# Optimization experiments

Hardware: AMD Instinct MI355X
Metric: run time of the kernel (lower is better)

The kernel has to match this reference:

```python
import jax, jax.numpy as jnp
import numpy as np

N0, N1, N2 = 100000, 50000, 20000
D = 128
E0, E1 = 600000, 300000


def _sage_rel(x_src, x_dst, src, dst, Ws, Wn, b, n_dst):
    """DGL SAGEConv(mean): fc_self(x_dst) + fc_neigh(mean of in-neighbors) + b."""
    msg = x_src[src]                                              # [E, D] gather
    ssum = jax.ops.segment_sum(msg, dst, num_segments=n_dst)      # [n_dst, D]
    deg = jax.ops.segment_sum(jnp.ones(dst.shape, x_src.dtype), dst, num_segments=n_dst)
    h_neigh = ssum / jnp.maximum(deg, 1.0)[:, None]               # zero-degree -> 0
    return x_dst @ Ws + h_neigh @ Wn + b


def setup_inputs() -> dict:
    key = jax.random.key(0)
    ks = jax.random.split(key, 24)
    p = 0.05
    inp = {
        "x": jax.random.normal(ks[0], (N0, D), jnp.float32),
        "e0_src_r0": jax.random.randint(ks[1], (E0,), 0, N0),
        "e0_dst_r0": jax.random.randint(ks[2], (E0,), 0, N1),
        "e0_src_r1": jax.random.randint(ks[3], (E0,), 0, N0),
        "e0_dst_r1": jax.random.randint(ks[4], (E0,), 0, N1),
        "e1_src_r0": jax.random.randint(ks[5], (E1,), 0, N1),
        "e1_dst_r0": jax.random.randint(ks[6], (E1,), 0, N2),
        "e1_src_r1": jax.random.randint(ks[7], (E1,), 0, N1),
        "e1_dst_r1": jax.random.randint(ks[8], (E1,), 0, N2),
    }
    names = ["Ws1_r0", "Wn1_r0", "Ws1_r1", "Wn1_r1", "Ws2_r0", "Wn2_r0", "Ws2_r1", "Wn2_r1"]
    for i, n in enumerate(names):
        inp[n] = jax.random.normal(ks[9 + i], (D, D), jnp.float32) * p
    for i, n in enumerate(["b1_r0", "b1_r1", "b2_r0", "b2_r1"]):
        inp[n] = jax.random.normal(ks[17 + i], (D,), jnp.float32) * p
    return inp


def reference(x, e0_src_r0, e0_dst_r0, e0_src_r1, e0_dst_r1,
              e1_src_r0, e1_dst_r0, e1_src_r1, e1_dst_r1,
              Ws1_r0, Wn1_r0, b1_r0, Ws1_r1, Wn1_r1, b1_r1,
              Ws2_r0, Wn2_r0, b2_r0, Ws2_r1, Wn2_r1, b2_r1):
    # Layer 1: HeteroGraphConv sum over relations, then ReLU
    x_dst1 = x[:N1]
    h1 = (_sage_rel(x, x_dst1, e0_src_r0, e0_dst_r0, Ws1_r0, Wn1_r0, b1_r0, N1)
          + _sage_rel(x, x_dst1, e0_src_r1, e0_dst_r1, Ws1_r1, Wn1_r1, b1_r1, N1))
    h1 = jax.nn.relu(h1)
    # Layer 2
    h1_dst = h1[:N2]
    h2 = (_sage_rel(h1, h1_dst, e1_src_r0, e1_dst_r0, Ws2_r0, Wn2_r0, b2_r0, N2)
          + _sage_rel(h1, h1_dst, e1_src_r1, e1_dst_r1, Ws2_r1, Wn2_r1, b2_r1, N2))
    return h2
```

## Files before the change

kernel.cpp:

```cpp
#include <hip/hip_runtime.h>
#include <hip/hip_bf16.h>

#define N0 100000
#define N1 50000
#define N2 20000
#define DD 128
#define E0 600000
#define E1 300000

#define NSEG_TOT (2 * N1 + 2 * N2)
#define ETOT     (2 * E0 + 2 * E1)

#define SEG_SHIFT 9
#define NBK  ((NSEG_TOT + 511) / 512)
#define NBK_PAD 288
#define CH   2048
#define NCH  ((ETOT + CH - 1) / CH)
#define CAP  13568

#define CAST_BLOCKS 12500
#define PREP_BLOCKS 48
#define CNT_BLOCKS  NCH
#define PROLOGUE_BLOCKS (CAST_BLOCKS + PREP_BLOCKS + CNT_BLOCKS)

typedef __attribute__((ext_vector_type(8))) short short8;
typedef __attribute__((ext_vector_type(4))) float floatx4;

__device__ __forceinline__ void st2bf(__hip_bfloat16* p, float a, float b) {
    __hip_bfloat162 v;
    v.x = __float2bfloat16(a);
    v.y = __float2bfloat16(b);
    *(__hip_bfloat162*)p = v;
}
__device__ __forceinline__ short bf16bits(float v) {
    __hip_bfloat16 b = __float2bfloat16(v);
    return *(short*)&b;
}
__device__ __forceinline__ float bf2f(unsigned short u) {
    return __uint_as_float(((unsigned int)u) << 16);
}
__device__ __forceinline__ float4 ld4bf(const __hip_bfloat16* p) {
    ushort4 u = *(const ushort4*)p;
    return make_float4(bf2f(u.x), bf2f(u.y), bf2f(u.z), bf2f(u.w));
}
__device__ __forceinline__ void st4bf(__hip_bfloat16* p, float4 v) {
    short vs[4];
    vs[0] = bf16bits(v.x); vs[1] = bf16bits(v.y);
    vs[2] = bf16bits(v.z); vs[3] = bf16bits(v.w);
    *(int2*)p = *(int2*)vs;
}

__device__ __forceinline__ int scan256(int s, int* sh, int t) {
    sh[t] = s;
    __syncthreads();
    for (int off = 1; off < 256; off <<= 1) {
        int tmp = (t >= off) ? sh[t - off] : 0;
        __syncthreads();
        sh[t] += tmp;
        __syncthreads();
    }
    return sh[t];
}

__device__ __forceinline__ int edge_seg(int e,
    const int* d0, const int* d1, const int* d2, const int* d3)
{
    if (e < E0)               return d0[e];
    if (e < 2 * E0)           return N1 + d1[e - E0];
    if (e < 2 * E0 + E1)      return 2 * N1 + d2[e - 2 * E0];
    return 2 * N1 + N2 + d3[e - 2 * E0 - E1];
}
__device__ __forceinline__ int2 edge_seg_src(int e,
    const int* s0, const int* d0, const int* s1, const int* d1,
    const int* s2, const int* d2, const int* s3, const int* d3)
{
    if (e < E0)               return make_int2(s0[e],            d0[e]);
    if (e < 2 * E0)           return make_int2(s1[e - E0],       N1 + d1[e - E0]);
    if (e < 2 * E0 + E1)      return make_int2(s2[e - 2 * E0],   2 * N1 + d2[e - 2 * E0]);
    int ee = e - 2 * E0 - E1;
    return make_int2(s3[ee], 2 * N1 + N2 + d3[ee]);
}

__global__ __launch_bounds__(256) void prologue_kernel(
    const float* __restrict__ x, __hip_bfloat16* __restrict__ xb,
    const int* __restrict__ d0a, const int* __restrict__ d0b,
    const int* __restrict__ d1a, const int* __restrict__ d1b,
    int* __restrict__ cntmat,
    const float* __restrict__ Ws1a, const float* __restrict__ Ws1b,
    const float* __restrict__ Wn1a, const float* __restrict__ Wn1b,
    const float* __restrict__ Ws2a, const float* __restrict__ Ws2b,
    const float* __restrict__ Wn2a, const float* __restrict__ Wn2b,
    short* __restrict__ wfrag1, short* __restrict__ wfrag2)
{
    __shared__ int hist[NBK_PAD];
    const int bid = blockIdx.x;
    const int t = threadIdx.x;
    if (bid < CAST_BLOCKS) {
        int i = bid * 256 + t;
        float4 v = ((const float4*)x)[i];
        st2bf(xb + (size_t)i * 4, v.x, v.y);
        st2bf(xb + (size_t)i * 4 + 2, v.z, v.w);
    } else if (bid < CAST_BLOCKS + PREP_BLOCKS) {
        int p = (bid - CAST_BLOCKS) * 256 + t;
        int layer = p >= 6144;
        int q = p - layer * 6144;
        int lane = q & 63;
        int mt = (q >> 6) & 7;
        int kc = q >> 9;
        int n = mt * 16 + (lane & 15);
        int k0 = kc * 32 + ((lane >> 4) << 3);
        const float* Wsa = layer ? Ws2a : Ws1a;
        const float* Wsb = layer ? Ws2b : Ws1b;
        const float* Wna = layer ? Wn2a : Wn1a;
        const float* Wnb = layer ? Wn2b : Wn1b;
        short* wf = layer ? wfrag2 : wfrag1;
        short vals[8];
#pragma unroll
        for (int j = 0; j < 8; j++) {
            int k = k0 + j;
            float w;
            if (k < 128)      w = Wsa[k * DD + n] + Wsb[k * DD + n];
            else if (k < 256) w = Wna[(k - 128) * DD + n];
            else              w = Wnb[(k - 256) * DD + n];
            vals[j] = bf16bits(w);
        }
        *(short8*)(wf + (size_t)q * 8) = *(short8*)vals;
    } else {
        const int chunk = bid - CAST_BLOCKS - PREP_BLOCKS;
        for (int l = t; l < NBK_PAD; l += 256) hist[l] = 0;
        __syncthreads();
#pragma unroll
        for (int it = 0; it < CH / 256; it++) {
            int e = chunk * CH + it * 256 + t;
            if (e < ETOT) {
                int seg = edge_seg(e, d0a, d0b, d1a, d1b);
                atomicAdd(&hist[seg >> SEG_SHIFT], 1);
            }
        }
        __syncthreads();
        for (int g = t; g < NBK; g += 256)
            cntmat[(size_t)g * NCH + chunk] = hist[g];
    }
}

__global__ __launch_bounds__(256) void scan_chunks_kernel(
    const int* __restrict__ cntmat, int* __restrict__ pre, int* __restrict__ tot)
{
    __shared__ int sh[256];
    const int t = threadIdx.x;
    const int g = blockIdx.x;
    const size_t roff = (size_t)g * NCH;
    int v[4]; int s = 0;
#pragma unroll
    for (int i = 0; i < 4; i++) {
        int idx = t * 4 + i;
        v[i] = (idx < NCH) ? cntmat[roff + idx] : 0;
        s += v[i];
    }
    int incl = scan256(s, sh, t);
    int ex = incl - s;
#pragma unroll
    for (int i = 0; i < 4; i++) {
        int idx = t * 4 + i;
        if (idx < NCH) pre[roff + idx] = ex;
        ex += v[i];
    }
    if (t == 255) tot[g] = incl;
}

__device__ __forceinline__ void build_base(const int* tot, int* basel, int* sh, int t)
{
    int l0 = 2 * t, l1 = 2 * t + 1;
    int v0 = (l0 < NBK) ? tot[l0] : 0;
    int v1 = (l1 < NBK) ? tot[l1] : 0;
    int s = v0 + v1;
    int incl = scan256(s, sh, t);
    int ex = incl - s;
    basel[l0] = ex;
    basel[l1] = ex + v0;
}

__global__ __launch_bounds__(256) void bucket_scatter_kernel(
    const int* __restrict__ s0a, const int* __restrict__ d0a,
    const int* __restrict__ s0b, const int* __restrict__ d0b,
    const int* __restrict__ s1a, const int* __restrict__ d1a,
    const int* __restrict__ s1b, const int* __restrict__ d1b,
    const int* __restrict__ pre, const int* __restrict__ tot,
    int2* __restrict__ ebuf)
{
    __shared__ int sh[256];
    __shared__ int basel[512];
    __shared__ int cur[NBK_PAD];
    const int t = threadIdx.x;
    const int chunk = blockIdx.x;

    build_base(tot, basel, sh, t);
    for (int l = t; l < NBK_PAD; l += 256) cur[l] = 0;
    __syncthreads();

#pragma unroll
    for (int it = 0; it < CH / 256; it++) {
        int e = chunk * CH + it * 256 + t;
        if (e < ETOT) {
            int2 r = edge_seg_src(e, s0a, d0a, s0b, d0b, s1a, d1a, s1b, d1b);
            int g = r.y >> SEG_SHIFT;
            int rk = atomicAdd(&cur[g], 1);
            int pos = basel[g] + pre[(size_t)g * NCH + chunk] + rk;
            ebuf[pos] = r;
        }
    }
}

__global__ __launch_bounds__(256) void csr_finalize_kernel(
    const int2* __restrict__ ebuf, const int* __restrict__ tot,
    int* __restrict__ row_ptr, int* __restrict__ eidx)
{
    __shared__ int sh[256];
    __shared__ int basel[512];
    __shared__ int cnt[512];
    __shared__ int excl[512];
    __shared__ int leidx[CAP];
    const int t = threadIdx.x;
    const int g = blockIdx.x;
    const int l0 = 2 * t, l1 = 2 * t + 1;

    build_base(tot, basel, sh, t);
    cnt[l0] = 0; cnt[l1] = 0;
    __syncthreads();

    const int b0 = basel[g];
    const int b1 = (g + 1 < 512) ? basel[g + 1] : ETOT;
    const int Eloc = b1 - b0;
    const int segbase = g << SEG_SHIFT;

    for (int i = t; i < Eloc; i += 256) {
        int2 rec = ebuf[b0 + i];
        atomicAdd(&cnt[rec.y - segbase], 1);
    }
    __syncthreads();

    int c0 = cnt[l0], c1 = cnt[l1];
    int ss = c0 + c1;
    int inc2 = scan256(ss, sh, t);
    int ex2 = inc2 - ss;
    excl[l0] = ex2;
    excl[l1] = ex2 + c0;
    __syncthreads();

    int nloc = NSEG_TOT - segbase;
    if (nloc > 512) nloc = 512;
    for (int l = t; l < nloc; l += 256) row_ptr[segbase + l] = b0 + excl[l];
    if (g == 0 && t == 0) row_ptr[NSEG_TOT] = ETOT;

    cnt[l0] = 0; cnt[l1] = 0;
    __syncthreads();

    if (Eloc <= CAP) {
        for (int i = t; i < Eloc; i += 256) {
            int2 rec = ebuf[b0 + i];
            int l = rec.y - segbase;
            int r = atomicAdd(&cnt[l], 1);
            leidx[excl[l] + r] = rec.x;
        }
        __syncthreads();
        for (int i = t; i < Eloc; i += 256) eidx[b0 + i] = leidx[i];
    } else {
        for (int i = t; i < Eloc; i += 256) {
            int2 rec = ebuf[b0 + i];
            int l = rec.y - segbase;
            int r = atomicAdd(&cnt[l], 1);
            eidx[b0 + excl[l] + r] = rec.x;
        }
    }
}

__global__ __launch_bounds__(256) void aggregate_kernel(
    const __hip_bfloat16* __restrict__ xb,
    const int* __restrict__ row_ptr,
    const int* __restrict__ eidx,
    __hip_bfloat16* __restrict__ hn,
    int nseg)
{
    int wid = (blockIdx.x * 256 + threadIdx.x) >> 6;
    const int lane = threadIdx.x & 63;
    if (wid >= nseg) return;
    wid = __builtin_amdgcn_readfirstlane(wid);

    const int beg = row_ptr[wid];
    const int end = row_ptr[wid + 1];
    const int cnt = end - beg;
    const int half = lane >> 5;
    const int l32 = lane & 31;

    float4 s = make_float4(0.f, 0.f, 0.f, 0.f);
    int k = beg;
    for (; k + 4 <= end; k += 4) {
        int i0 = eidx[k + 0];
        int i1 = eidx[k + 1];
        int i2 = eidx[k + 2];
        int i3 = eidx[k + 3];
        int ra = half ? i1 : i0;
        int rb = half ? i3 : i2;
        float4 va = ld4bf(xb + (long)ra * DD + l32 * 4);
        float4 vb = ld4bf(xb + (long)rb * DD + l32 * 4);
        s.x += va.x + vb.x; s.y += va.y + vb.y;
        s.z += va.z + vb.z; s.w += va.w + vb.w;
    }
    if (k + 2 <= end) {
        int i0 = eidx[k];
        int i1 = eidx[k + 1];
        int r = half ? i1 : i0;
        float4 v = ld4bf(xb + (long)r * DD + l32 * 4);
        s.x += v.x; s.y += v.y; s.z += v.z; s.w += v.w;
        k += 2;
    }
    if (k < end && !half) {
        int i0 = eidx[k];
        float4 v = ld4bf(xb + (long)i0 * DD + l32 * 4);
        s.x += v.x; s.y += v.y; s.z += v.z; s.w += v.w;
    }

    s.x += __shfl_xor(s.x, 32);
    s.y += __shfl_xor(s.y, 32);
    s.z += __shfl_xor(s.z, 32);
    s.w += __shfl_xor(s.w, 32);

    if (!half) {
        const float inv = 1.f / (float)(cnt > 1 ? cnt : 1);
        float4 m = make_float4(s.x * inv, s.y * inv, s.z * inv, s.w * inv);
        st4bf(hn + (long)wid * DD + l32 * 4, m);
    }
}

template <bool RELU, typename TOUT>
__global__ __launch_bounds__(256) void mfma_combine_kernel(
    const __hip_bfloat16* __restrict__ xself,
    const __hip_bfloat16* __restrict__ hn,
    const short* __restrict__ wfrag,
    const float* __restrict__ b0, const float* __restrict__ b1,
    TOUT* __restrict__ out, int M)
{
    const int t = threadIdx.x;
    const int wave = t >> 6;
    const int lane = t & 63;
    const int nsub = lane & 15;
    const int quad = lane >> 4;
    const int base = blockIdx.x * 128 + wave * 32;

    const int node0 = base + nsub;
    const int node1 = base + 16 + nsub;
    const long n0c = node0 < M ? node0 : M - 1;
    const long n1c = node1 < M ? node1 : M - 1;

    floatx4 acc[2][8];
#pragma unroll
    for (int nt = 0; nt < 2; nt++)
#pragma unroll
        for (int mt = 0; mt < 8; mt++) acc[nt][mt] = (floatx4){0.f, 0.f, 0.f, 0.f};

    for (int kc = 0; kc < 12; kc++) {
        const __hip_bfloat16* src;
        long r0, r1;
        int koff;
        if (kc < 4)      { src = xself; koff = kc * 32;       r0 = n0c;     r1 = n1c; }
        else if (kc < 8) { src = hn;    koff = (kc - 4) * 32; r0 = n0c;     r1 = n1c; }
        else             { src = hn;    koff = (kc - 8) * 32; r0 = M + n0c; r1 = M + n1c; }

        short8 bf0 = *(const short8*)(src + r0 * DD + koff + quad * 8);
        short8 bf1 = *(const short8*)(src + r1 * DD + koff + quad * 8);
        const short* wbase = wfrag + ((size_t)(kc * 8) * 64 + lane) * 8;
#pragma unroll
        for (int mt = 0; mt < 8; mt++) {
            short8 af = *(const short8*)(wbase + (size_t)mt * 64 * 8);
            acc[0][mt] = __builtin_amdgcn_mfma_f32_16x16x32_bf16(af, bf0, acc[0][mt], 0, 0, 0);
            acc[1][mt] = __builtin_amdgcn_mfma_f32_16x16x32_bf16(af, bf1, acc[1][mt], 0, 0, 0);
        }
    }

#pragma unroll
    for (int nt = 0; nt < 2; nt++) {
        int node = (nt == 0) ? node0 : node1;
        if (node >= M) continue;
#pragma unroll
        for (int mt = 0; mt < 8; mt++) {
            int c0 = mt * 16 + quad * 4;
            float4 bb0 = *(const float4*)(b0 + c0);
            float4 bb1 = *(const float4*)(b1 + c0);
            float v0 = acc[nt][mt][0] + bb0.x + bb1.x;
            float v1 = acc[nt][mt][1] + bb0.y + bb1.y;
            float v2 = acc[nt][mt][2] + bb0.z + bb1.z;
            float v3 = acc[nt][mt][3] + bb0.w + bb1.w;
            if (RELU) {
                v0 = v0 > 0.f ? v0 : 0.f;
                v1 = v1 > 0.f ? v1 : 0.f;
                v2 = v2 > 0.f ? v2 : 0.f;
                v3 = v3 > 0.f ? v3 : 0.f;
            }
            TOUT* p = out + (long)node * DD + c0;
            if constexpr (sizeof(TOUT) == 4) {
                *(float4*)p = make_float4(v0, v1, v2, v3);
            } else {
                short vs[4];
                vs[0] = bf16bits(v0); vs[1] = bf16bits(v1);
                vs[2] = bf16bits(v2); vs[3] = bf16bits(v3);
                *(int2*)p = *(int2*)vs;
            }
        }
    }
}


extern "C" void kernel_launch(void* const* d_in, const int* in_sizes, int n_in,
                              void* d_out, int out_size, void* d_ws, size_t ws_size,
                              hipStream_t stream)
{
    const float* x = (const float*)d_in[0];
    const int* e0_src_r0 = (const int*)d_in[1];
    const int* e0_dst_r0 = (const int*)d_in[2];
    const int* e0_src_r1 = (const int*)d_in[3];
    const int* e0_dst_r1 = (const int*)d_in[4];
    const int* e1_src_r0 = (const int*)d_in[5];
    const int* e1_dst_r0 = (const int*)d_in[6];
    const int* e1_src_r1 = (const int*)d_in[7];
    const int* e1_dst_r1 = (const int*)d_in[8];
    const float* Ws1_r0 = (const float*)d_in[9];
    const float* Wn1_r0 = (const float*)d_in[10];
    const float* Ws1_r1 = (const float*)d_in[11];
    const float* Wn1_r1 = (const float*)d_in[12];
    const float* Ws2_r0 = (const float*)d_in[13];
    const float* Wn2_r0 = (const float*)d_in[14];
    const float* Ws2_r1 = (const float*)d_in[15];
    const float* Wn2_r1 = (const float*)d_in[16];
    const float* b1_r0 = (const float*)d_in[17];
    const float* b1_r1 = (const float*)d_in[18];
    const float* b2_r0 = (const float*)d_in[19];
    const float* b2_r1 = (const float*)d_in[20];
    float* out = (float*)d_out;

    __hip_bfloat16* xb = (__hip_bfloat16*)d_ws;
    __hip_bfloat16* h1 = xb;
    __hip_bfloat16* hn = xb + (size_t)N0 * DD;
    int2* ebuf    = (int2*)hn;
    int* eidx     = (int*)(hn + (size_t)2 * N1 * DD);
    int* row_ptr  = eidx + ETOT;
    int* cntmat   = row_ptr + NSEG_TOT + 4;
    int* pre      = cntmat + NBK * NCH;
    int* tot      = pre + NBK * NCH;
    short* wfrag1 = (short*)(tot + NBK + 4);
    short* wfrag2 = wfrag1 + 12 * 8 * 64 * 8;

    prologue_kernel<<<PROLOGUE_BLOCKS, 256, 0, stream>>>(
        x, xb,
        e0_dst_r0, e0_dst_r1, e1_dst_r0, e1_dst_r1,
        cntmat,
        Ws1_r0, Ws1_r1, Wn1_r0, Wn1_r1,
        Ws2_r0, Ws2_r1, Wn2_r0, Wn2_r1,
        wfrag1, wfrag2);

    scan_chunks_kernel<<<NBK, 256, 0, stream>>>(cntmat, pre, tot);

    bucket_scatter_kernel<<<NCH, 256, 0, stream>>>(
        e0_src_r0, e0_dst_r0, e0_src_r1, e0_dst_r1,
        e1_src_r0, e1_dst_r0, e1_src_r1, e1_dst_r1,
        pre, tot, ebuf);

    csr_finalize_kernel<<<NBK, 256, 0, stream>>>(ebuf, tot, row_ptr, eidx);

    aggregate_kernel<<<(2 * N1 + 3) / 4, 256, 0, stream>>>(xb, row_ptr, eidx, hn, 2 * N1);
    mfma_combine_kernel<true, __hip_bfloat16>
        <<<(N1 + 127) / 128, 256, 0, stream>>>(xb, hn, wfrag1, b1_r0, b1_r1, h1, N1);

    aggregate_kernel<<<(2 * N2 + 3) / 4, 256, 0, stream>>>(h1, row_ptr + 2 * N1, eidx, hn, 2 * N2);
    mfma_combine_kernel<false, float>
        <<<(N2 + 127) / 128, 256, 0, stream>>>(h1, hn, wfrag2, b2_r0, b2_r1, out, N2);
}
```

Baseline: 297.1 us.

## Fuse CSR build into cooperative kernel and fuse aggregation with MFMA combine

Merges the prologue, chunk scan, bucket scatter and CSR finalize into one cooperative kernel with grid syncs, replacing four launches. It also fuses neighbor aggregation with the MFMA linear layer per layer, keeping mean features in LDS instead of writing and rereading them through global memory. The finalize step drops the LDS staging of eidx and writes scattered to global. The fused layer uses 64 nodes per block with one N-tile per wave, which halves weight reuse per fragment load, and grid syncs plus the fixed 1024-block grid may limit parallelism in the cast and scatter phases.

Result: slower. 828.1 us (+178.8%).

```diff
diff --git a/kernel.cpp b/kernel.cpp
--- a/kernel.cpp
+++ b/kernel.cpp
@@ -1,5 +1,8 @@
 #include <hip/hip_runtime.h>
+#include <hip/hip_cooperative_groups.h>
 #include <hip/hip_bf16.h>
+
+namespace cg = cooperative_groups;
 
 #define N0 100000
 #define N1 50000
@@ -16,12 +19,12 @@
 #define NBK_PAD 288
 #define CH   2048
 #define NCH  ((ETOT + CH - 1) / CH)
-#define CAP  13568
-
-#define CAST_BLOCKS 12500
-#define PREP_BLOCKS 48
-#define CNT_BLOCKS  NCH
-#define PROLOGUE_BLOCKS (CAST_BLOCKS + PREP_BLOCKS + CNT_BLOCKS)
+
+#define COOP_GRID 1024
+
+#define LNODES 64
+#define LROWS  (2 * LNODES)
+#define LSTRIDE 152
 
 typedef __attribute__((ext_vector_type(8))) short short8;
 typedef __attribute__((ext_vector_type(4))) float floatx4;
@@ -79,93 +82,6 @@
     if (e < 2 * E0 + E1)      return make_int2(s2[e - 2 * E0],   2 * N1 + d2[e - 2 * E0]);
     int ee = e - 2 * E0 - E1;
     return make_int2(s3[ee], 2 * N1 + N2 + d3[ee]);
-}
-
-__global__ __launch_bounds__(256) void prologue_kernel(
-    const float* __restrict__ x, __hip_bfloat16* __restrict__ xb,
-    const int* __restrict__ d0a, const int* __restrict__ d0b,
-    const int* __restrict__ d1a, const int* __restrict__ d1b,
-    int* __restrict__ cntmat,
-    const float* __restrict__ Ws1a, const float* __restrict__ Ws1b,
-    const float* __restrict__ Wn1a, const float* __restrict__ Wn1b,
-    const float* __restrict__ Ws2a, const float* __restrict__ Ws2b,
-    const float* __restrict__ Wn2a, const float* __restrict__ Wn2b,
-    short* __restrict__ wfrag1, short* __restrict__ wfrag2)
-{
-    __shared__ int hist[NBK_PAD];
-    const int bid = blockIdx.x;
-    const int t = threadIdx.x;
-    if (bid < CAST_BLOCKS) {
-        int i = bid * 256 + t;
-        float4 v = ((const float4*)x)[i];
-        st2bf(xb + (size_t)i * 4, v.x, v.y);
-        st2bf(xb + (size_t)i * 4 + 2, v.z, v.w);
-    } else if (bid < CAST_BLOCKS + PREP_BLOCKS) {
-        int p = (bid - CAST_BLOCKS) * 256 + t;
-        int layer = p >= 6144;
-        int q = p - layer * 6144;
-        int lane = q & 63;
-        int mt = (q >> 6) & 7;
-        int kc = q >> 9;
-        int n = mt * 16 + (lane & 15);
-        int k0 = kc * 32 + ((lane >> 4) << 3);
-        const float* Wsa = layer ? Ws2a : Ws1a;
-        const float* Wsb = layer ? Ws2b : Ws1b;
-        const float* Wna = layer ? Wn2a : Wn1a;
-        const float* Wnb = layer ? Wn2b : Wn1b;
-        short* wf = layer ? wfrag2 : wfrag1;
-        short vals[8];
-#pragma unroll
-        for (int j = 0; j < 8; j++) {
-            int k = k0 + j;
-            float w;
-            if (k < 128)      w = Wsa[k * DD + n] + Wsb[k * DD + n];
-            else if (k < 256) w = Wna[(k - 128) * DD + n];
-            else              w = Wnb[(k - 256) * DD + n];
-            vals[j] = bf16bits(w);
-        }
-        *(short8*)(wf + (size_t)q * 8) = *(short8*)vals;
-    } else {
-        const int chunk = bid - CAST_BLOCKS - PREP_BLOCKS;
-        for (int l = t; l < NBK_PAD; l += 256) hist[l] = 0;
-        __syncthreads();
-#pragma unroll
-        for (int it = 0; it < CH / 256; it++) {
-            int e = chunk * CH + it * 256 + t;
-            if (e < ETOT) {
-                int seg = edge_seg(e, d0a, d0b, d1a, d1b);
-                atomicAdd(&hist[seg >> SEG_SHIFT], 1);
-            }
-        }
-        __syncthreads();
-        for (int g = t; g < NBK; g += 256)
-            cntmat[(size_t)g * NCH + chunk] = hist[g];
-    }
-}
-
-__global__ __launch_bounds__(256) void scan_chunks_kernel(
-    const int* __restrict__ cntmat, int* __restrict__ pre, int* __restrict__ tot)
-{
-    __shared__ int sh[256];
-    const int t = threadIdx.x;
-    const int g = blockIdx.x;
-    const size_t roff = (size_t)g * NCH;
-    int v[4]; int s = 0;
-#pragma unroll
-    for (int i = 0; i < 4; i++) {
-        int idx = t * 4 + i;
-        v[i] = (idx < NCH) ? cntmat[roff + idx] : 0;
-        s += v[i];
-    }
-    int incl = scan256(s, sh, t);
-    int ex = incl - s;
-#pragma unroll
-    for (int i = 0; i < 4; i++) {
-        int idx = t * 4 + i;
-        if (idx < NCH) pre[roff + idx] = ex;
-        ex += v[i];
-    }
-    if (t == 255) tot[g] = incl;
 }
 
 __device__ __forceinline__ void build_base(const int* tot, int* basel, int* sh, int t)
@@ -180,216 +96,262 @@
     basel[l1] = ex + v0;
 }
 
-__global__ __launch_bounds__(256) void bucket_scatter_kernel(
-    const int* __restrict__ s0a, const int* __restrict__ d0a,
-    const int* __restrict__ s0b, const int* __restrict__ d0b,
-    const int* __restrict__ s1a, const int* __restrict__ d1a,
-    const int* __restrict__ s1b, const int* __restrict__ d1b,
-    const int* __restrict__ pre, const int* __restrict__ tot,
-    int2* __restrict__ ebuf)
-{
+struct CsrArgs {
+    const float* x; __hip_bfloat16* xb;
+    const int* s0a; const int* d0a; const int* s0b; const int* d0b;
+    const int* s1a; const int* d1a; const int* s1b; const int* d1b;
+    int* cntmat; int* pre; int* tot; int2* ebuf; int* row_ptr; int* eidx;
+    const float* Ws1a; const float* Ws1b; const float* Wn1a; const float* Wn1b;
+    const float* Ws2a; const float* Ws2b; const float* Wn2a; const float* Wn2b;
+    short* wfrag1; short* wfrag2;
+};
+
+__global__ __launch_bounds__(256, 4) void coop_csr_kernel(CsrArgs a)
+{
+    cg::grid_group grid = cg::this_grid();
     __shared__ int sh[256];
     __shared__ int basel[512];
-    __shared__ int cur[NBK_PAD];
+    __shared__ int hist[512];
+    __shared__ int excl[512];
     const int t = threadIdx.x;
-    const int chunk = blockIdx.x;
-
-    build_base(tot, basel, sh, t);
-    for (int l = t; l < NBK_PAD; l += 256) cur[l] = 0;
+    const int nthr = gridDim.x * 256;
+    const int gtid = blockIdx.x * 256 + t;
+
+    for (int i = gtid; i < N0 * DD / 4; i += nthr) {
+        float4 v = ((const float4*)a.x)[i];
+        st2bf(a.xb + (size_t)i * 4, v.x, v.y);
+        st2bf(a.xb + (size_t)i * 4 + 2, v.z, v.w);
+    }
+    for (int p = gtid; p < 2 * 6144; p += nthr) {
+        int layer = p >= 6144;
+        int q = p - layer * 6144;
+        int lane = q & 63;
+        int mt = (q >> 6) & 7;
+        int kc = q >> 9;
+        int n = mt * 16 + (lane & 15);
+        int k0 = kc * 32 + ((lane >> 4) << 3);
+        const float* Wsa = layer ? a.Ws2a : a.Ws1a;
+        const float* Wsb = layer ? a.Ws2b : a.Ws1b;
+        const float* Wna = layer ? a.Wn2a : a.Wn1a;
+        const float* Wnb = layer ? a.Wn2b : a.Wn1b;
+        short* wf = layer ? a.wfrag2 : a.wfrag1;
+        short vals[8];
+#pragma unroll
+        for (int j = 0; j < 8; j++) {
+            int k = k0 + j;
+            float w;
+            if (k < 128)      w = Wsa[k * DD + n] + Wsb[k * DD + n];
+            else if (k < 256) w = Wna[(k - 128) * DD + n];
+            else              w = Wnb[(k - 256) * DD + n];
+            vals[j] = bf16bits(w);
+        }
+        *(short8*)(wf + (size_t)q * 8) = *(short8*)vals;
+    }
+    for (int chunk = blockIdx.x; chunk < NCH; chunk += gridDim.x) {
+        for (int l = t; l < NBK_PAD; l += 256) hist[l] = 0;
+        __syncthreads();
+#pragma unroll
+        for (int it = 0; it < CH / 256; it++) {
+            int e = chunk * CH + it * 256 + t;
+            if (e < ETOT) {
+                int seg = edge_seg(e, a.d0a, a.d0b, a.d1a, a.d1b);
+                atomicAdd(&hist[seg >> SEG_SHIFT], 1);
+            }
+        }
+        __syncthreads();
+        for (int g = t; g < NBK; g += 256)
+            a.cntmat[(size_t)g * NCH + chunk] = hist[g];
+        __syncthreads();
+    }
+    grid.sync();
+
+    for (int g = blockIdx.x; g < NBK; g += gridDim.x) {
+        const size_t roff = (size_t)g * NCH;
+        int v[4]; int s = 0;
+#pragma unroll
+        for (int i = 0; i < 4; i++) {
+            int idx = t * 4 + i;
+            v[i] = (idx < NCH) ? a.cntmat[roff + idx] : 0;
+            s += v[i];
+        }
+        int incl = scan256(s, sh, t);
+        int ex = incl - s;
+#pragma unroll
+        for (int i = 0; i < 4; i++) {
+            int idx = t * 4 + i;
+            if (idx < NCH) a.pre[roff + idx] = ex;
+            ex += v[i];
+        }
+        if (t == 255) a.tot[g] = incl;
+        __syncthreads();
+    }
+    grid.sync();
+
+    build_base(a.tot, basel, sh, t);
     __syncthreads();
-
-#pragma unroll
-    for (int it = 0; it < CH / 256; it++) {
-        int e = chunk * CH + it * 256 + t;
-        if (e < ETOT) {
-            int2 r = edge_seg_src(e, s0a, d0a, s0b, d0b, s1a, d1a, s1b, d1b);
-            int g = r.y >> SEG_SHIFT;
-            int rk = atomicAdd(&cur[g], 1);
-            int pos = basel[g] + pre[(size_t)g * NCH + chunk] + rk;
-            ebuf[pos] = r;
-        }
-    }
-}
-
-__global__ __launch_bounds__(256) void csr_finalize_kernel(
-    const int2* __restrict__ ebuf, const int* __restrict__ tot,
-    int* __restrict__ row_ptr, int* __restrict__ eidx)
-{
-    __shared__ int sh[256];
-    __shared__ int basel[512];
-    __shared__ int cnt[512];
-    __shared__ int excl[512];
-    __shared__ int leidx[CAP];
-    const int t = threadIdx.x;
-    const int g = blockIdx.x;
+    for (int chunk = blockIdx.x; chunk < NCH; chunk += gridDim.x) {
+        for (int l = t; l < NBK_PAD; l += 256) hist[l] = 0;
+        __syncthreads();
+#pragma unroll
+        for (int it = 0; it < CH / 256; it++) {
+            int e = chunk * CH + it * 256 + t;
+            if (e < ETOT) {
+                int2 r = edge_seg_src(e, a.s0a, a.d0a, a.s0b, a.d0b,
+                                         a.s1a, a.d1a, a.s1b, a.d1b);
+                int g = r.y >> SEG_SHIFT;
+                int rk = atomicAdd(&hist[g], 1);
+                a.ebuf[basel[g] + a.pre[(size_t)g * NCH + chunk] + rk] = r;
+            }
+        }
+        __syncthreads();
+    }
+    grid.sync();
+
     const int l0 = 2 * t, l1 = 2 * t + 1;
-
-    build_base(tot, basel, sh, t);
-    cnt[l0] = 0; cnt[l1] = 0;
-    __syncthreads();
-
-    const int b0 = basel[g];
-    const int b1 = (g + 1 < 512) ? basel[g + 1] : ETOT;
-    const int Eloc = b1 - b0;
-    const int segbase = g << SEG_SHIFT;
-
-    for (int i = t; i < Eloc; i += 256) {
-        int2 rec = ebuf[b0 + i];
-        atomicAdd(&cnt[rec.y - segbase], 1);
-    }
-    __syncthreads();
-
-    int c0 = cnt[l0], c1 = cnt[l1];
-    int ss = c0 + c1;
-    int inc2 = scan256(ss, sh, t);
-    int ex2 = inc2 - ss;
-    excl[l0] = ex2;
-    excl[l1] = ex2 + c0;
-    __syncthreads();
-
-    int nloc = NSEG_TOT - segbase;
-    if (nloc > 512) nloc = 512;
-    for (int l = t; l < nloc; l += 256) row_ptr[segbase + l] = b0 + excl[l];
-    if (g == 0 && t == 0) row_ptr[NSEG_TOT] = ETOT;
-
-    cnt[l0] = 0; cnt[l1] = 0;
-    __syncthreads();
-
-    if (Eloc <= CAP) {
+    for (int g = blockIdx.x; g < NBK; g += gridDim.x) {
+        hist[l0] = 0; hist[l1] = 0;
+        __syncthreads();
+        const int b0 = basel[g];
+        const int b1 = basel[g + 1];
+        const int Eloc = b1 - b0;
+        const int segbase = g << SEG_SHIFT;
+
         for (int i = t; i < Eloc; i += 256) {
-            int2 rec = ebuf[b0 + i];
+            int2 rec = a.ebuf[b0 + i];
+            atomicAdd(&hist[rec.y - segbase], 1);
+        }
+        __syncthreads();
+
+        int c0 = hist[l0], c1 = hist[l1];
+        int ssum = c0 + c1;
+        int inc2 = scan256(ssum, sh, t);
+        int ex2 = inc2 - ssum;
+        excl[l0] = ex2;
+        excl[l1] = ex2 + c0;
+        __syncthreads();
+
+        int nloc = NSEG_TOT - segbase;
+        if (nloc > 512) nloc = 512;
+        for (int l = t; l < nloc; l += 256) a.row_ptr[segbase + l] = b0 + excl[l];
+        if (g == 0 && t == 0) a.row_ptr[NSEG_TOT] = ETOT;
+
+        hist[l0] = 0; hist[l1] = 0;
+        __syncthreads();
+
+        for (int i = t; i < Eloc; i += 256) {
+            int2 rec = a.ebuf[b0 + i];
             int l = rec.y - segbase;
-            int r = atomicAdd(&cnt[l], 1);
-            leidx[excl[l] + r] = rec.x;
-        }
-        __syncthreads();
-        for (int i = t; i < Eloc; i += 256) eidx[b0 + i] = leidx[i];
-    } else {
-        for (int i = t; i < Eloc; i += 256) {
-            int2 rec = ebuf[b0 + i];
-            int l = rec.y - segbase;
-            int r = atomicAdd(&cnt[l], 1);
-            eidx[b0 + excl[l] + r] = rec.x;
-        }
-    }
-}
-
-__global__ __launch_bounds__(256) void aggregate_kernel(
-    const __hip_bfloat16* __restrict__ xb,
+            int r = atomicAdd(&hist[l], 1);
+            a.eidx[b0 + excl[l] + r] = rec.x;
+        }
+        __syncthreads();
+    }
+}
+
+template <bool RELU, typename TOUT>
+__global__ __launch_bounds__(256) void fused_layer_kernel(
+    const __hip_bfloat16* __restrict__ xsrc,
     const int* __restrict__ row_ptr,
     const int* __restrict__ eidx,
-    __hip_bfloat16* __restrict__ hn,
-    int nseg)
-{
-    int wid = (blockIdx.x * 256 + threadIdx.x) >> 6;
-    const int lane = threadIdx.x & 63;
-    if (wid >= nseg) return;
-    wid = __builtin_amdgcn_readfirstlane(wid);
-
-    const int beg = row_ptr[wid];
-    const int end = row_ptr[wid + 1];
-    const int cnt = end - beg;
-    const int half = lane >> 5;
-    const int l32 = lane & 31;
-
-    float4 s = make_float4(0.f, 0.f, 0.f, 0.f);
-    int k = beg;
-    for (; k + 4 <= end; k += 4) {
-        int i0 = eidx[k + 0];
-        int i1 = eidx[k + 1];
-        int i2 = eidx[k + 2];
-        int i3 = eidx[k + 3];
-        int ra = half ? i1 : i0;
-        int rb = half ? i3 : i2;
-        float4 va = ld4bf(xb + (long)ra * DD + l32 * 4);
-        float4 vb = ld4bf(xb + (long)rb * DD + l32 * 4);
-        s.x += va.x + vb.x; s.y += va.y + vb.y;
-        s.z += va.z + vb.z; s.w += va.w + vb.w;
-    }
-    if (k + 2 <= end) {
-        int i0 = eidx[k];
-        int i1 = eidx[k + 1];
-        int r = half ? i1 : i0;
-        float4 v = ld4bf(xb + (long)r * DD + l32 * 4);
-        s.x += v.x; s.y += v.y; s.z += v.z; s.w += v.w;
-        k += 2;
-    }
-    if (k < end && !half) {
-        int i0 = eidx[k];
-        float4 v = ld4bf(xb + (long)i0 * DD + l32 * 4);
-        s.x += v.x; s.y += v.y; s.z += v.z; s.w += v.w;
-    }
-
-    s.x += __shfl_xor(s.x, 32);
-    s.y += __shfl_xor(s.y, 32);
-    s.z += __shfl_xor(s.z, 32);
-    s.w += __shfl_xor(s.w, 32);
-
-    if (!half) {
-        const float inv = 1.f / (float)(cnt > 1 ? cnt : 1);
-        float4 m = make_float4(s.x * inv, s.y * inv, s.z * inv, s.w * inv);
-        st4bf(hn + (long)wid * DD + l32 * 4, m);
-    }
-}
-
-template <bool RELU, typename TOUT>
-__global__ __launch_bounds__(256) void mfma_combine_kernel(
-    const __hip_bfloat16* __restrict__ xself,
-    const __hip_bfloat16* __restrict__ hn,
     const short* __restrict__ wfrag,
     const float* __restrict__ b0, const float* __restrict__ b1,
     TOUT* __restrict__ out, int M)
 {
+    __shared__ __align__(16) short lhn[LROWS * LSTRIDE];
     const int t = threadIdx.x;
     const int wave = t >> 6;
     const int lane = t & 63;
+    const int nb0 = blockIdx.x * LNODES;
+
+    const int half = lane >> 5;
+    const int l32 = lane & 31;
+    for (int li = wave * 32; li < wave * 32 + 32; li++) {
+        int rel = li >> 6;
+        int node = nb0 + (li & 63);
+        float4 s = make_float4(0.f, 0.f, 0.f, 0.f);
+        int cnt = 0;
+        if (node < M) {
+            int seg = rel * M + node;
+            int beg = row_ptr[seg];
+            int end = row_ptr[seg + 1];
+            cnt = end - beg;
+            int k = beg;
+            for (; k + 4 <= end; k += 4) {
+                int i0 = eidx[k + 0];
+                int i1 = eidx[k + 1];
+                int i2 = eidx[k + 2];
+                int i3 = eidx[k + 3];
+                int ra = half ? i1 : i0;
+                int rb = half ? i3 : i2;
+                float4 va = ld4bf(xsrc + (long)ra * DD + l32 * 4);
+                float4 vb = ld4bf(xsrc + (long)rb * DD + l32 * 4);
+                s.x += va.x + vb.x; s.y += va.y + vb.y;
+                s.z += va.z + vb.z; s.w += va.w + vb.w;
+            }
+            if (k + 2 <= end) {
+                int i0 = eidx[k];
+                int i1 = eidx[k + 1];
+                int r = half ? i1 : i0;
+                float4 v = ld4bf(xsrc + (long)r * DD + l32 * 4);
+                s.x += v.x; s.y += v.y; s.z += v.z; s.w += v.w;
+                k += 2;
+            }
+            if (k < end && !half) {
+                int i0 = eidx[k];
+                float4 v = ld4bf(xsrc + (long)i0 * DD + l32 * 4);
+                s.x += v.x; s.y += v.y; s.z += v.z; s.w += v.w;
+            }
+        }
+        s.x += __shfl_xor(s.x, 32);
+        s.y += __shfl_xor(s.y, 32);
+        s.z += __shfl_xor(s.z, 32);
+        s.w += __shfl_xor(s.w, 32);
+        if (!half) {
+            const float inv = 1.f / (float)(cnt > 1 ? cnt : 1);
+            st4bf((__hip_bfloat16*)&lhn[li * LSTRIDE + l32 * 4],
+                  make_float4(s.x * inv, s.y * inv, s.z * inv, s.w * inv));
+        }
+    }
+    __syncthreads();
+
     const int nsub = lane & 15;
     const int quad = lane >> 4;
-    const int base = blockIdx.x * 128 + wave * 32;
-
-    const int node0 = base + nsub;
-    const int node1 = base + 16 + nsub;
-    const long n0c = node0 < M ? node0 : M - 1;
-    const long n1c = node1 < M ? node1 : M - 1;
-
-    floatx4 acc[2][8];
-#pragma unroll
-    for (int nt = 0; nt < 2; nt++)
-#pragma unroll
-        for (int mt = 0; mt < 8; mt++) acc[nt][mt] = (floatx4){0.f, 0.f, 0.f, 0.f};
+    const int lnode = wave * 16 + nsub;
+    const int node = nb0 + lnode;
+    const long nc = node < M ? node : M - 1;
+
+    floatx4 acc[8];
+#pragma unroll
+    for (int mt = 0; mt < 8; mt++) acc[mt] = (floatx4){0.f, 0.f, 0.f, 0.f};
 
     for (int kc = 0; kc < 12; kc++) {
-        const __hip_bfloat16* src;
-        long r0, r1;
-        int koff;
-        if (kc < 4)      { src = xself; koff = kc * 32;       r0 = n0c;     r1 = n1c; }
-        else if (kc < 8) { src = hn;    koff = (kc - 4) * 32; r0 = n0c;     r1 = n1c; }
-        else             { src = hn;    koff = (kc - 8) * 32; r0 = M + n0c; r1 = M + n1c; }
-
-        short8 bf0 = *(const short8*)(src + r0 * DD + koff + quad * 8);
-        short8 bf1 = *(const short8*)(src + r1 * DD + koff + quad * 8);
+        short8 bf;
+        if (kc < 4) {
+            bf = *(const short8*)(xsrc + nc * DD + kc * 32 + quad * 8);
+        } else {
+            int rel = (kc >= 8);
+            int koff = (kc - 4 - rel * 4) * 32;
+            int li = rel * LNODES + lnode;
+            bf = *(const short8*)(lhn + li * LSTRIDE + koff + quad * 8);
+        }
         const short* wbase = wfrag + ((size_t)(kc * 8) * 64 + lane) * 8;
 #pragma unroll
         for (int mt = 0; mt < 8; mt++) {
             short8 af = *(const short8*)(wbase + (size_t)mt * 64 * 8);
-            acc[0][mt] = __builtin_amdgcn_mfma_f32_16x16x32_bf16(af, bf0, acc[0][mt], 0, 0, 0);
-            acc[1][mt] = __builtin_amdgcn_mfma_f32_16x16x32_bf16(af, bf1, acc[1][mt], 0, 0, 0);
-        }
-    }
-
-#pragma unroll
-    for (int nt = 0; nt < 2; nt++) {
-        int node = (nt == 0) ? node0 : node1;
-        if (node >= M) continue;
+            acc[mt] = __builtin_amdgcn_mfma_f32_16x16x32_bf16(af, bf, acc[mt], 0, 0, 0);
+        }
+    }
+
+    if (node < M) {
 #pragma unroll
         for (int mt = 0; mt < 8; mt++) {
             int c0 = mt * 16 + quad * 4;
             float4 bb0 = *(const float4*)(b0 + c0);
             float4 bb1 = *(const float4*)(b1 + c0);
-            float v0 = acc[nt][mt][0] + bb0.x + bb1.x;
-            float v1 = acc[nt][mt][1] + bb0.y + bb1.y;
-            float v2 = acc[nt][mt][2] + bb0.z + bb1.z;
-            float v3 = acc[nt][mt][3] + bb0.w + bb1.w;
+            float v0 = acc[mt][0] + bb0.x + bb1.x;
+            float v1 = acc[mt][1] + bb0.y + bb1.y;
+            float v2 = acc[mt][2] + bb0.z + bb1.z;
+            float v3 = acc[mt][3] + bb0.w + bb1.w;
             if (RELU) {
                 v0 = v0 > 0.f ? v0 : 0.f;
                 v1 = v1 > 0.f ? v1 : 0.f;
@@ -438,10 +400,9 @@
     float* out = (float*)d_out;
 
     __hip_bfloat16* xb = (__hip_bfloat16*)d_ws;
-    __hip_bfloat16* h1 = xb;
-    __hip_bfloat16* hn = xb + (size_t)N0 * DD;
-    int2* ebuf    = (int2*)hn;
-    int* eidx     = (int*)(hn + (size_t)2 * N1 * DD);
+    __hip_bfloat16* h1 = xb + (size_t)N0 * DD;
+    int2* ebuf    = (int2*)(h1 + (size_t)N1 * DD);
+    int* eidx     = (int*)(ebuf + ETOT);
     int* row_ptr  = eidx + ETOT;
     int* cntmat   = row_ptr + NSEG_TOT + 4;
     int* pre      = cntmat + NBK * NCH;
@@ -449,28 +410,24 @@
     short* wfrag1 = (short*)(tot + NBK + 4);
     short* wfrag2 = wfrag1 + 12 * 8 * 64 * 8;
 
-    prologue_kernel<<<PROLOGUE_BLOCKS, 256, 0, stream>>>(
-        x, xb,
-        e0_dst_r0, e0_dst_r1, e1_dst_r0, e1_dst_r1,
-        cntmat,
-        Ws1_r0, Ws1_r1, Wn1_r0, Wn1_r1,
-        Ws2_r0, Ws2_r1, Wn2_r0, Wn2_r1,
-        wfrag1, wfrag2);
-
-    scan_chunks_kernel<<<NBK, 256, 0, stream>>>(cntmat, pre, tot);
-
-    bucket_scatter_kernel<<<NCH, 256, 0, stream>>>(
-        e0_src_r0, e0_dst_r0, e0_src_r1, e0_dst_r1,
-        e1_src_r0, e1_dst_r0, e1_src_r1, e1_dst_r1,
-        pre, tot, ebuf);
-
-    csr_finalize_kernel<<<NBK, 256, 0, stream>>>(ebuf, tot, row_ptr, eidx);
-
-    aggregate_kernel<<<(2 * N1 + 3) / 4, 256, 0, stream>>>(xb, row_ptr, eidx, hn, 2 * N1);
-    mfma_combine_kernel<true, __hip_bfloat16>
-        <<<(N1 + 127) / 128, 256, 0, stream>>>(xb, hn, wfrag1, b1_r0, b1_r1, h1, N1);
-
-    aggregate_kernel<<<(2 * N2 + 3) / 4, 256, 0, stream>>>(h1, row_ptr + 2 * N1, eidx, hn, 2 * N2);
-    mfma_combine_kernel<false, float>
-        <<<(N2 + 127) / 128, 256, 0, stream>>>(h1, hn, wfrag2, b2_r0, b2_r1, out, N2);
-}
+    CsrArgs ca;
+    ca.x = x; ca.xb = xb;
+    ca.s0a = e0_src_r0; ca.d0a = e0_dst_r0; ca.s0b = e0_src_r1; ca.d0b = e0_dst_r1;
+    ca.s1a = e1_src_r0; ca.d1a = e1_dst_r0; ca.s1b = e1_src_r1; ca.d1b = e1_dst_r1;
+    ca.cntmat = cntmat; ca.pre = pre; ca.tot = tot; ca.ebuf = ebuf;
+    ca.row_ptr = row_ptr; ca.eidx = eidx;
+    ca.Ws1a = Ws1_r0; ca.Ws1b = Ws1_r1; ca.Wn1a = Wn1_r0; ca.Wn1b = Wn1_r1;
+    ca.Ws2a = Ws2_r0; ca.Ws2b = Ws2_r1; ca.Wn2a = Wn2_r0; ca.Wn2b = Wn2_r1;
+    ca.wfrag1 = wfrag1; ca.wfrag2 = wfrag2;
+    void* args[] = { &ca };
+    hipLaunchCooperativeKernel((const void*)coop_csr_kernel,
+                               dim3(COOP_GRID), dim3(256), args, 0, stream);
+
+    fused_layer_kernel<true, __hip_bfloat16>
+        <<<(N1 + LNODES - 1) / LNODES, 256, 0, stream>>>(
+            xb, row_ptr, eidx, wfrag1, b1_r0, b1_r1, h1, N1);
+
+    fused_layer_kernel<false, float>
+        <<<(N2 + LNODES - 1) / LNODES, 256, 0, stream>>>(
+            h1, row_ptr + 2 * N1, eidx, wfrag2, b2_r0, b2_r1, out, N2);
+}
```

## Fuse bucket scatter into prologue via chunk-local sort, drop scatter kernel

Applied to the files above, without the earlier changes.

Each prologue chunk block now reads its edges once, builds a bucket histogram and local offsets, and writes its edges sorted by bucket into a chunk-local buffer. The CSR finalize kernel then gathers each bucket's runs from every chunk into shared memory using the count, offset and prefix matrices. This removes the separate bucket_scatter kernel and its second pass over the source and destination arrays. In exchange it adds an extra offset matrix, a large shared-memory staging array in the prologue that may limit occupancy of the cast blocks, and a per-thread serial gather in finalize.

After: 282.9 us. -4.8%, faster.

```diff
diff --git a/kernel.cpp b/kernel.cpp
--- a/kernel.cpp
+++ b/kernel.cpp
@@ -13,15 +13,13 @@
 
 #define SEG_SHIFT 9
 #define NBK  ((NSEG_TOT + 511) / 512)
-#define NBK_PAD 288
 #define CH   2048
 #define NCH  ((ETOT + CH - 1) / CH)
-#define CAP  13568
+#define CAP_REC 8192
 
 #define CAST_BLOCKS 12500
 #define PREP_BLOCKS 48
-#define CNT_BLOCKS  NCH
-#define PROLOGUE_BLOCKS (CAST_BLOCKS + PREP_BLOCKS + CNT_BLOCKS)
+#define PROLOGUE_BLOCKS (CAST_BLOCKS + PREP_BLOCKS + NCH)
 
 typedef __attribute__((ext_vector_type(8))) short short8;
 typedef __attribute__((ext_vector_type(4))) float floatx4;
@@ -62,14 +60,6 @@
     return sh[t];
 }
 
-__device__ __forceinline__ int edge_seg(int e,
-    const int* d0, const int* d1, const int* d2, const int* d3)
-{
-    if (e < E0)               return d0[e];
-    if (e < 2 * E0)           return N1 + d1[e - E0];
-    if (e < 2 * E0 + E1)      return 2 * N1 + d2[e - 2 * E0];
-    return 2 * N1 + N2 + d3[e - 2 * E0 - E1];
-}
 __device__ __forceinline__ int2 edge_seg_src(int e,
     const int* s0, const int* d0, const int* s1, const int* d1,
     const int* s2, const int* d2, const int* s3, const int* d3)
@@ -81,20 +71,39 @@
     return make_int2(s3[ee], 2 * N1 + N2 + d3[ee]);
 }
 
+__device__ __forceinline__ void build_base(const int* tot, int* basel, int* sh, int t)
+{
+    int l0 = 2 * t, l1 = 2 * t + 1;
+    int v0 = (l0 < NBK) ? tot[l0] : 0;
+    int v1 = (l1 < NBK) ? tot[l1] : 0;
+    int s = v0 + v1;
+    int incl = scan256(s, sh, t);
+    int ex = incl - s;
+    basel[l0] = ex;
+    basel[l1] = ex + v0;
+}
+
 __global__ __launch_bounds__(256) void prologue_kernel(
     const float* __restrict__ x, __hip_bfloat16* __restrict__ xb,
-    const int* __restrict__ d0a, const int* __restrict__ d0b,
-    const int* __restrict__ d1a, const int* __restrict__ d1b,
-    int* __restrict__ cntmat,
+    const int* __restrict__ s0a, const int* __restrict__ d0a,
+    const int* __restrict__ s0b, const int* __restrict__ d0b,
+    const int* __restrict__ s1a, const int* __restrict__ d1a,
+    const int* __restrict__ s1b, const int* __restrict__ d1b,
+    int* __restrict__ cntmat, int* __restrict__ ofsmat,
+    int2* __restrict__ chunkbuf,
     const float* __restrict__ Ws1a, const float* __restrict__ Ws1b,
     const float* __restrict__ Wn1a, const float* __restrict__ Wn1b,
     const float* __restrict__ Ws2a, const float* __restrict__ Ws2b,
     const float* __restrict__ Wn2a, const float* __restrict__ Wn2b,
     short* __restrict__ wfrag1, short* __restrict__ wfrag2)
 {
-    __shared__ int hist[NBK_PAD];
+    __shared__ int hist[512];
+    __shared__ int ofs[512];
+    __shared__ int sh[256];
+    __shared__ int2 rec[CH];
     const int bid = blockIdx.x;
     const int t = threadIdx.x;
+
     if (bid < CAST_BLOCKS) {
         int i = bid * 256 + t;
         float4 v = ((const float4*)x)[i];
@@ -127,19 +136,52 @@
         *(short8*)(wf + (size_t)q * 8) = *(short8*)vals;
     } else {
         const int chunk = bid - CAST_BLOCKS - PREP_BLOCKS;
-        for (int l = t; l < NBK_PAD; l += 256) hist[l] = 0;
-        __syncthreads();
+        const int ebase = chunk * CH;
+        const int ecount = (ETOT - ebase < CH) ? (ETOT - ebase) : CH;
+
+        hist[t] = 0; hist[t + 256] = 0;
+        __syncthreads();
+
+        int2 myrec[CH / 256];
 #pragma unroll
         for (int it = 0; it < CH / 256; it++) {
-            int e = chunk * CH + it * 256 + t;
+            int e = ebase + it * 256 + t;
+            int2 r = make_int2(0, -1);
             if (e < ETOT) {
-                int seg = edge_seg(e, d0a, d0b, d1a, d1b);
-                atomicAdd(&hist[seg >> SEG_SHIFT], 1);
-            }
-        }
-        __syncthreads();
-        for (int g = t; g < NBK; g += 256)
+                r = edge_seg_src(e, s0a, d0a, s0b, d0b, s1a, d1a, s1b, d1b);
+                atomicAdd(&hist[r.y >> SEG_SHIFT], 1);
+            }
+            myrec[it] = r;
+        }
+        __syncthreads();
+
+        const int l0 = 2 * t, l1 = 2 * t + 1;
+        int c0 = hist[l0], c1 = hist[l1];
+        int s = c0 + c1;
+        int incl = scan256(s, sh, t);
+        int ex = incl - s;
+        ofs[l0] = ex;
+        ofs[l1] = ex + c0;
+        __syncthreads();
+
+        for (int g = t; g < NBK; g += 256) {
             cntmat[(size_t)g * NCH + chunk] = hist[g];
+            ofsmat[(size_t)g * NCH + chunk] = ofs[g];
+        }
+        __syncthreads();
+
+#pragma unroll
+        for (int it = 0; it < CH / 256; it++) {
+            int2 r = myrec[it];
+            if (r.y >= 0) {
+                int rk = atomicAdd(&ofs[r.y >> SEG_SHIFT], 1);
+                rec[rk] = r;
+            }
+        }
+        __syncthreads();
+
+        for (int i = t; i < ecount; i += 256)
+            chunkbuf[ebase + i] = rec[i];
     }
 }
 
@@ -168,58 +210,17 @@
     if (t == 255) tot[g] = incl;
 }
 
-__device__ __forceinline__ void build_base(const int* tot, int* basel, int* sh, int t)
-{
-    int l0 = 2 * t, l1 = 2 * t + 1;
-    int v0 = (l0 < NBK) ? tot[l0] : 0;
-    int v1 = (l1 < NBK) ? tot[l1] : 0;
-    int s = v0 + v1;
-    int incl = scan256(s, sh, t);
-    int ex = incl - s;
-    basel[l0] = ex;
-    basel[l1] = ex + v0;
-}
-
-__global__ __launch_bounds__(256) void bucket_scatter_kernel(
-    const int* __restrict__ s0a, const int* __restrict__ d0a,
-    const int* __restrict__ s0b, const int* __restrict__ d0b,
-    const int* __restrict__ s1a, const int* __restrict__ d1a,
-    const int* __restrict__ s1b, const int* __restrict__ d1b,
+__global__ __launch_bounds__(256) void csr_finalize_kernel(
+    const int2* __restrict__ chunkbuf,
+    const int* __restrict__ cntmat, const int* __restrict__ ofsmat,
     const int* __restrict__ pre, const int* __restrict__ tot,
-    int2* __restrict__ ebuf)
-{
-    __shared__ int sh[256];
-    __shared__ int basel[512];
-    __shared__ int cur[NBK_PAD];
-    const int t = threadIdx.x;
-    const int chunk = blockIdx.x;
-
-    build_base(tot, basel, sh, t);
-    for (int l = t; l < NBK_PAD; l += 256) cur[l] = 0;
-    __syncthreads();
-
-#pragma unroll
-    for (int it = 0; it < CH / 256; it++) {
-        int e = chunk * CH + it * 256 + t;
-        if (e < ETOT) {
-            int2 r = edge_seg_src(e, s0a, d0a, s0b, d0b, s1a, d1a, s1b, d1b);
-            int g = r.y >> SEG_SHIFT;
-            int rk = atomicAdd(&cur[g], 1);
-            int pos = basel[g] + pre[(size_t)g * NCH + chunk] + rk;
-            ebuf[pos] = r;
-        }
-    }
-}
-
-__global__ __launch_bounds__(256) void csr_finalize_kernel(
-    const int2* __restrict__ ebuf, const int* __restrict__ tot,
     int* __restrict__ row_ptr, int* __restrict__ eidx)
 {
     __shared__ int sh[256];
     __shared__ int basel[512];
     __shared__ int cnt[512];
     __shared__ int excl[512];
-    __shared__ int leidx[CAP];
+    __shared__ int2 rec[CAP_REC];
     const int t = threadIdx.x;
     const int g = blockIdx.x;
     const int l0 = 2 * t, l1 = 2 * t + 1;
@@ -229,20 +230,40 @@
     __syncthreads();
 
     const int b0 = basel[g];
-    const int b1 = (g + 1 < 512) ? basel[g + 1] : ETOT;
+    const int b1 = basel[g + 1];
     const int Eloc = b1 - b0;
     const int segbase = g << SEG_SHIFT;
-
-    for (int i = t; i < Eloc; i += 256) {
-        int2 rec = ebuf[b0 + i];
-        atomicAdd(&cnt[rec.y - segbase], 1);
+    const bool fits = (Eloc <= CAP_REC);
+
+    if (fits) {
+        for (int c = t; c < NCH; c += 256) {
+            size_t m = (size_t)g * NCH + c;
+            int len = cntmat[m];
+            int off = ofsmat[m];
+            int dst = pre[m];
+            for (int i = 0; i < len; i++)
+                rec[dst + i] = chunkbuf[c * CH + off + i];
+        }
+        __syncthreads();
+        for (int i = t; i < Eloc; i += 256)
+            atomicAdd(&cnt[rec[i].y - segbase], 1);
+    } else {
+        for (int c = t; c < NCH; c += 256) {
+            size_t m = (size_t)g * NCH + c;
+            int len = cntmat[m];
+            int off = ofsmat[m];
+            for (int i = 0; i < len; i++) {
+                int2 r = chunkbuf[c * CH + off + i];
+                atomicAdd(&cnt[r.y - segbase], 1);
+            }
+        }
     }
     __syncthreads();
 
     int c0 = cnt[l0], c1 = cnt[l1];
-    int ss = c0 + c1;
-    int inc2 = scan256(ss, sh, t);
-    int ex2 = inc2 - ss;
+    int ssum = c0 + c1;
+    int inc2 = scan256(ssum, sh, t);
+    int ex2 = inc2 - ssum;
     excl[l0] = ex2;
     excl[l1] = ex2 + c0;
     __syncthreads();
@@ -255,21 +276,24 @@
     cnt[l0] = 0; cnt[l1] = 0;
     __syncthreads();
 
-    if (Eloc <= CAP) {
+    if (fits) {
         for (int i = t; i < Eloc; i += 256) {
-            int2 rec = ebuf[b0 + i];
-            int l = rec.y - segbase;
-            int r = atomicAdd(&cnt[l], 1);
-            leidx[excl[l] + r] = rec.x;
-        }
-        __syncthreads();
-        for (int i = t; i < Eloc; i += 256) eidx[b0 + i] = leidx[i];
+            int2 r = rec[i];
+            int l = r.y - segbase;
+            int rk = atomicAdd(&cnt[l], 1);
+            eidx[b0 + excl[l] + rk] = r.x;
+        }
     } else {
-        for (int i = t; i < Eloc; i += 256) {
-            int2 rec = ebuf[b0 + i];
-            int l = rec.y - segbase;
-            int r = atomicAdd(&cnt[l], 1);
-            eidx[b0 + excl[l] + r] = rec.x;
+        for (int c = t; c < NCH; c += 256) {
+            size_t m = (size_t)g * NCH + c;
+            int len = cntmat[m];
+            int off = ofsmat[m];
+            for (int i = 0; i < len; i++) {
+                int2 r = chunkbuf[c * CH + off + i];
+                int l = r.y - segbase;
+                int rk = atomicAdd(&cnt[l], 1);
+                eidx[b0 + excl[l] + rk] = r.x;
+            }
         }
     }
 }
@@ -440,31 +464,29 @@
     __hip_bfloat16* xb = (__hip_bfloat16*)d_ws;
     __hip_bfloat16* h1 = xb;
     __hip_bfloat16* hn = xb + (size_t)N0 * DD;
-    int2* ebuf    = (int2*)hn;
+    int2* chunkbuf = (int2*)hn;
     int* eidx     = (int*)(hn + (size_t)2 * N1 * DD);
     int* row_ptr  = eidx + ETOT;
     int* cntmat   = row_ptr + NSEG_TOT + 4;
-    int* pre      = cntmat + NBK * NCH;
+    int* ofsmat   = cntmat + NBK * NCH;
+    int* pre      = ofsmat + NBK * NCH;
     int* tot      = pre + NBK * NCH;
     short* wfrag1 = (short*)(tot + NBK + 4);
     short* wfrag2 = wfrag1 + 12 * 8 * 64 * 8;
 
     prologue_kernel<<<PROLOGUE_BLOCKS, 256, 0, stream>>>(
         x, xb,
-        e0_dst_r0, e0_dst_r1, e1_dst_r0, e1_dst_r1,
-        cntmat,
+        e0_src_r0, e0_dst_r0, e0_src_r1, e0_dst_r1,
+        e1_src_r0, e1_dst_r0, e1_src_r1, e1_dst_r1,
+        cntmat, ofsmat, chunkbuf,
         Ws1_r0, Ws1_r1, Wn1_r0, Wn1_r1,
         Ws2_r0, Ws2_r1, Wn2_r0, Wn2_r1,
         wfrag1, wfrag2);
 
     scan_chunks_kernel<<<NBK, 256, 0, stream>>>(cntmat, pre, tot);
 
-    bucket_scatter_kernel<<<NCH, 256, 0, stream>>>(
-        e0_src_r0, e0_dst_r0, e0_src_r1, e0_dst_r1,
-        e1_src_r0, e1_dst_r0, e1_src_r1, e1_dst_r1,
-        pre, tot, ebuf);
-
-    csr_finalize_kernel<<<NBK, 256, 0, stream>>>(ebuf, tot, row_ptr, eidx);
+    csr_finalize_kernel<<<NBK, 256, 0, stream>>>(
+        chunkbuf, cntmat, ofsmat, pre, tot, row_ptr, eidx);
 
     aggregate_kernel<<<(2 * N1 + 3) / 4, 256, 0, stream>>>(xb, row_ptr, eidx, hn, 2 * N1);
     mfma_combine_kernel<true, __hip_bfloat16>
```
